# Performance work log

Hardware: AMD Instinct MI355X
Metric: run time of the kernel (lower is better)

## Reference

```python
import jax, jax.numpy as jnp
import numpy as np

D_HIDDEN = 400
D_ANCHOR = 31
N_LAYER = 24
N_HEADS = 8
DIM_HEAD = 400
D_INNER = 800
D_STATE = 16
D_CONV = 4
DT_RANK = 25  # ceil(400/16)
PE_HIDDEN = 48
EPS = 1e-5


def _point_embed(x, w, b):
    # Fourier point embedding (3DShape2VecSet PointEmbed), dim-major freq layout.
    d = x.shape[-1]
    nf = PE_HIDDEN // (2 * d)
    freqs = (2.0 ** jnp.arange(nf, dtype=x.dtype)) * jnp.pi  # [nf]
    proj = (x[..., None] * freqs).reshape(*x.shape[:-1], d * nf)  # [b,n,d*nf]
    emb = jnp.concatenate([jnp.sin(proj), jnp.cos(proj), x], axis=-1)  # [b,n,48+d]
    return emb @ w.T + b


def _rmsnorm(x, w):
    return x * jax.lax.rsqrt(jnp.mean(x * x, axis=-1, keepdims=True) + EPS) * w


def _layernorm(x, w, b):
    mu = jnp.mean(x, axis=-1, keepdims=True)
    var = jnp.var(x, axis=-1, keepdims=True)
    return (x - mu) * jax.lax.rsqrt(var + EPS) * w + b


def _selective_scan(u, dt, A, Bm, Cm, Dp):
    # u, dt: [b,l,di]; A: [di,n]; Bm, Cm: [b,l,n]; Dp: [di]
    def step(h, inp):
        u_t, dt_t, B_t, C_t = inp  # [b,di],[b,di],[b,n],[b,n]
        h = jnp.exp(dt_t[..., None] * A) * h + (dt_t * u_t)[..., None] * B_t[:, None, :]
        return h, jnp.einsum('bdn,bn->bd', h, C_t)
    h0 = jnp.zeros((u.shape[0], u.shape[2], A.shape[1]), u.dtype)
    xs = (jnp.swapaxes(u, 0, 1), jnp.swapaxes(dt, 0, 1),
          jnp.swapaxes(Bm, 0, 1), jnp.swapaxes(Cm, 0, 1))
    _, ys = jax.lax.scan(step, h0, xs)
    return jnp.swapaxes(ys, 0, 1) + u * Dp


def _mamba_block(x, norm_w, in_w, conv_w, conv_b, xproj_w, dt_w, dt_b, A_log, Dp, out_w):
    b, L, _ = x.shape
    xn = _rmsnorm(x, norm_w)
    u, z = jnp.split(xn @ in_w.T, 2, axis=-1)  # each [b,L,di]
    # causal depthwise conv1d, kernel D_CONV, left pad D_CONV-1 (torch conv truncated to L)
    u_pad = jnp.pad(u, ((0, 0), (D_CONV - 1, 0), (0, 0)))
    conv = sum(u_pad[:, k:k + L, :] * conv_w[:, k] for k in range(D_CONV)) + conv_b
    u_c = jax.nn.silu(conv)
    dbc = u_c @ xproj_w.T  # [b,L,dt_rank+2n]
    dt, Bm, Cm = jnp.split(dbc, [DT_RANK, DT_RANK + D_STATE], axis=-1)
    dt = jax.nn.softplus(dt @ dt_w.T + dt_b)  # [b,L,di]
    y = _selective_scan(u_c, dt, -jnp.exp(A_log), Bm, Cm, Dp)
    return x + (y * jax.nn.silu(z)) @ out_w.T


def _forward(mash_params, qry, anchor_w, anchor_b, point_w, point_b,
             norm_w, in_w, conv_w, conv_b, xproj_w, dt_w, dt_b, A_log, Dp, out_w,
             ln_q_w, ln_q_b, ln_c_w, ln_c_b, to_q_w, to_kv_w, to_out_w, to_out_b,
             ff_ln_w, ff_ln_b, ff_w1, ff_b1, ff_w2, ff_b2, head_w, head_b):
    # anchor embed on first 6 dims, concat remaining 25 -> [b,na,400]
    anc = _point_embed(mash_params[:, :, :6], anchor_w, anchor_b)
    x = jnp.concatenate([anc, mash_params[:, :, 6:]], axis=-1)
    for i in range(N_LAYER):
        x = _mamba_block(x, norm_w[i], in_w[i], conv_w[i], conv_b[i], xproj_w[i],
                         dt_w[i], dt_b[i], A_log[i], Dp[i], out_w[i])
    q_emb = _point_embed(qry, point_w, point_b)  # [b,nq,400]
    # PreNorm cross-attention (query norm + context norm), no residual
    qn = _layernorm(q_emb, ln_q_w, ln_q_b)
    ctx = _layernorm(x, ln_c_w, ln_c_b)
    b, nq, _ = qn.shape
    na = ctx.shape[1]
    q = (qn @ to_q_w.T).reshape(b, nq, N_HEADS, DIM_HEAD)
    k, v = jnp.split(ctx @ to_kv_w.T, 2, axis=-1)
    k = k.reshape(b, na, N_HEADS, DIM_HEAD)
    v = v.reshape(b, na, N_HEADS, DIM_HEAD)
    sim = jnp.einsum('bihd,bjhd->bhij', q, k) * (DIM_HEAD ** -0.5)
    attn = jax.nn.softmax(sim, axis=-1)
    out = jnp.einsum('bhij,bjhd->bihd', attn, v).reshape(b, nq, N_HEADS * DIM_HEAD)
    latents = out @ to_out_w.T + to_out_b  # [b,nq,400]
    # PreNorm GEGLU FeedForward with residual
    h = _layernorm(latents, ff_ln_w, ff_ln_b) @ ff_w1.T + ff_b1  # [b,nq,3200]
    a, g = jnp.split(h, 2, axis=-1)
    h = (a * jax.nn.gelu(g)) @ ff_w2.T + ff_b2
    latents = latents + h
    occ = (latents @ head_w.T + head_b).squeeze(-1)  # [b,nq]
    return occ


def setup_inputs() -> dict:
    key = jax.random.key(0)
    ks = iter(jax.random.split(key, 48))
    def nrm(shape, scale=0.02):
        return jax.random.normal(next(ks), shape, dtype=jnp.float32) * scale
    B, NA, NQ = 4, 400, 4096
    INNER = N_HEADS * DIM_HEAD  # 3200
    dt_init = jax.random.uniform(next(ks), (N_LAYER, D_INNER), minval=1e-3, maxval=0.1)
    inp = {
        'mash_params': nrm((B, NA, D_ANCHOR), 1.0),
        'qry': jax.random.uniform(next(ks), (B, NQ, 3), minval=-1.0, maxval=1.0),
        'anchor_w': nrm((D_HIDDEN - D_ANCHOR + 6, PE_HIDDEN + 6)),
        'anchor_b': jnp.zeros((D_HIDDEN - D_ANCHOR + 6,), jnp.float32),
        'point_w': nrm((D_HIDDEN, PE_HIDDEN + 3)),
        'point_b': jnp.zeros((D_HIDDEN,), jnp.float32),
        'norm_w': jnp.ones((N_LAYER, D_HIDDEN), jnp.float32),
        'in_w': nrm((N_LAYER, 2 * D_INNER, D_HIDDEN)),
        'conv_w': nrm((N_LAYER, D_INNER, D_CONV), 0.2),
        'conv_b': jnp.zeros((N_LAYER, D_INNER), jnp.float32),
        'xproj_w': nrm((N_LAYER, DT_RANK + 2 * D_STATE, D_INNER)),
        'dt_w': nrm((N_LAYER, D_INNER, DT_RANK), 0.1),
        'dt_b': jnp.log(jnp.expm1(dt_init)),
        'A_log': jnp.log(jnp.broadcast_to(jnp.arange(1, D_STATE + 1, dtype=jnp.float32),
                                          (N_LAYER, D_INNER, D_STATE))),
        'Dp': jnp.ones((N_LAYER, D_INNER), jnp.float32),
        'out_w': nrm((N_LAYER, D_HIDDEN, D_INNER)),
        'ln_q_w': jnp.ones((D_HIDDEN,), jnp.float32), 'ln_q_b': jnp.zeros((D_HIDDEN,), jnp.float32),
        'ln_c_w': jnp.ones((D_HIDDEN,), jnp.float32), 'ln_c_b': jnp.zeros((D_HIDDEN,), jnp.float32),
        'to_q_w': nrm((INNER, D_HIDDEN)),
        'to_kv_w': nrm((2 * INNER, D_HIDDEN)),
        'to_out_w': nrm((D_HIDDEN, INNER)),
        'to_out_b': jnp.zeros((D_HIDDEN,), jnp.float32),
        'ff_ln_w': jnp.ones((D_HIDDEN,), jnp.float32), 'ff_ln_b': jnp.zeros((D_HIDDEN,), jnp.float32),
        'ff_w1': nrm((8 * D_HIDDEN, D_HIDDEN)),
        'ff_b1': jnp.zeros((8 * D_HIDDEN,), jnp.float32),
        'ff_w2': nrm((D_HIDDEN, 4 * D_HIDDEN)),
        'ff_b2': jnp.zeros((D_HIDDEN,), jnp.float32),
        'head_w': nrm((1, D_HIDDEN)),
        'head_b': jnp.zeros((1,), jnp.float32),
    }
    return inp


def reference(mash_params, qry, anchor_w, anchor_b, point_w, point_b,
              norm_w, in_w, conv_w, conv_b, xproj_w, dt_w, dt_b, A_log, Dp, out_w,
              ln_q_w, ln_q_b, ln_c_w, ln_c_b, to_q_w, to_kv_w, to_out_w, to_out_b,
              ff_ln_w, ff_ln_b, ff_w1, ff_b1, ff_w2, ff_b2, head_w, head_b):
    return _forward(mash_params, qry, anchor_w, anchor_b, point_w, point_b,
                    norm_w, in_w, conv_w, conv_b, xproj_w, dt_w, dt_b, A_log, Dp, out_w,
                    ln_q_w, ln_q_b, ln_c_w, ln_c_b, to_q_w, to_kv_w, to_out_w, to_out_b,
                    ff_ln_w, ff_ln_b, ff_w1, ff_b1, ff_w2, ff_b2, head_w, head_b)
```

## Files before the change

### kernel.cpp

```cpp
#include <hip/hip_runtime.h>


#define EPI_NONE 0
#define EPI_SOFTPLUS 1
#define EPI_RES 2
#define EPI_GEGLU 3

typedef short bf16x8 __attribute__((ext_vector_type(8)));
typedef float f32x4 __attribute__((ext_vector_type(4)));

static __device__ __forceinline__ float silu_f(float x) {
  return x / (1.f + __expf(-x));
}
static __device__ __forceinline__ float softplus_f(float x) {
  return fmaxf(x, 0.f) + log1pf(__expf(-fabsf(x)));
}
static __device__ __forceinline__ float gelu_f(float x) {
  const float c = 0.7978845608028654f;
  return 0.5f * x * (1.f + tanhf(c * (x + 0.044715f * x * x * x)));
}
static __device__ __forceinline__ unsigned short f2bf(float f) {
  union { float f; unsigned int u; } v; v.f = f;
  unsigned int r = v.u + 0x7FFFu + ((v.u >> 16) & 1u);
  return (unsigned short)(r >> 16);
}
static __device__ __forceinline__ float bf2f(unsigned short h) {
  union { unsigned int u; float f; } v; v.u = ((unsigned int)h) << 16;
  return v.f;
}

__global__ void cvt_w_kernel(const float* __restrict__ src, unsigned short* __restrict__ dst,
                             int Lr, int R, int C, int Rp, int Cp) {
  size_t i8 = ((size_t)blockIdx.x * 256 + threadIdx.x) * 8;
  size_t total = (size_t)Lr * Rp * Cp;
  if (i8 >= total) return;
  int cp = (int)(i8 % Cp);
  size_t rl = i8 / Cp;
  int r = (int)(rl % Rp);
  int l = (int)(rl / Rp);
  const float* s = src + ((size_t)l * R + r) * C + cp;
  bf16x8 o;
#pragma unroll
  for (int q = 0; q < 8; ++q) {
    float v = (r < R && (cp + q) < C) ? s[q] : 0.f;
    o[q] = (short)f2bf(v);
  }
  *reinterpret_cast<bf16x8*>(dst + i8) = o;
}

__global__ void cvt_headrow_k(const float* __restrict__ src, unsigned short* __restrict__ dst,
                              int HB) {
  size_t i8 = ((size_t)blockIdx.x * 256 + threadIdx.x) * 8;
  size_t total = (size_t)HB * 416 * 416;
  if (i8 >= total) return;
  int c = (int)(i8 % 416);
  int n = (int)(i8 / 416);
  int head = n / 416, r = n % 416;
  const float* s = src + ((size_t)(head * 400 + r)) * 400 + c;
  bf16x8 o;
#pragma unroll
  for (int q = 0; q < 8; ++q) {
    float v = (r < 400 && (c + q) < 400) ? s[q] : 0.f;
    o[q] = (short)f2bf(v);
  }
  *reinterpret_cast<bf16x8*>(dst + i8) = o;
}

__global__ void cvt_colhead_k(const float* __restrict__ src, unsigned short* __restrict__ dst,
                              int HB) {
  size_t i8 = ((size_t)blockIdx.x * 256 + threadIdx.x) * 8;
  size_t total = (size_t)512 * HB * 416;
  if (i8 >= total) return;
  int cp = (int)(i8 % ((size_t)HB * 416));
  int r = (int)(i8 / ((size_t)HB * 416));
  int head = cp / 416, cc = cp % 416;
  bf16x8 o;
#pragma unroll
  for (int q = 0; q < 8; ++q) {
    int c = cc + q;
    float v = (r < 400 && c < 400) ? src[(size_t)r * (HB * 400) + head * 400 + c] : 0.f;
    o[q] = (short)f2bf(v);
  }
  *reinterpret_cast<bf16x8*>(dst + i8) = o;
}

template <int EPI, int OUTBF>
__global__ __launch_bounds__(256) void gemm_bf16_k(
    const unsigned short* __restrict__ A, int lda, long long zsA,
    const unsigned short* __restrict__ W, int ldw, long long zsW,
    const float* __restrict__ bias,
    const float* __restrict__ aux, int ldaux,
    void* __restrict__ Cout, int ldc, long long zsC,
    int M, int N, int K) {
  __shared__ unsigned short As[128 * 32];
  __shared__ unsigned short Bs[128 * 32];
  const int tid = threadIdx.x;
  const int lane = tid & 63;
  const int wid = tid >> 6;
  const int wr = wid >> 1, wc = wid & 1;
  const int m0 = blockIdx.y * 128, n0 = blockIdx.x * 128;
  const long long z = blockIdx.z;
  A += z * zsA;
  W += z * zsW;

  f32x4 acc[4][4];
#pragma unroll
  for (int i = 0; i < 4; ++i)
#pragma unroll
    for (int j = 0; j < 4; ++j) acc[i][j] = (f32x4){0.f, 0.f, 0.f, 0.f};

  const int i0 = tid;
  const int i1 = tid + 256;
  const unsigned short* gA0 = A + (size_t)(m0 + (i0 >> 2)) * lda + ((i0 & 3) << 3);
  const unsigned short* gA1 = A + (size_t)(m0 + (i1 >> 2)) * lda + ((i1 & 3) << 3);
  const unsigned short* gB0 = W + (size_t)(n0 + (i0 >> 2)) * ldw + ((i0 & 3) << 3);
  const unsigned short* gB1 = W + (size_t)(n0 + (i1 >> 2)) * ldw + ((i1 & 3) << 3);
  unsigned short* lA0 = &As[i0 * 8];
  unsigned short* lA1 = &As[i1 * 8];
  unsigned short* lB0 = &Bs[i0 * 8];
  unsigned short* lB1 = &Bs[i1 * 8];

  const int fr = lane & 15, fq = lane >> 4;
  const int arow = wr * 64 + fr;
  const int brow = wc * 64 + fr;

  for (int k0 = 0; k0 < K; k0 += 32) {
    __builtin_amdgcn_global_load_lds(
        (const __attribute__((address_space(1))) unsigned int*)(gA0 + k0),
        (__attribute__((address_space(3))) unsigned int*)lA0, 16, 0, 0);
    __builtin_amdgcn_global_load_lds(
        (const __attribute__((address_space(1))) unsigned int*)(gA1 + k0),
        (__attribute__((address_space(3))) unsigned int*)lA1, 16, 0, 0);
    __builtin_amdgcn_global_load_lds(
        (const __attribute__((address_space(1))) unsigned int*)(gB0 + k0),
        (__attribute__((address_space(3))) unsigned int*)lB0, 16, 0, 0);
    __builtin_amdgcn_global_load_lds(
        (const __attribute__((address_space(1))) unsigned int*)(gB1 + k0),
        (__attribute__((address_space(3))) unsigned int*)lB1, 16, 0, 0);
    __syncthreads();
    bf16x8 av[4], bv[4];
#pragma unroll
    for (int mi = 0; mi < 4; ++mi)
      av[mi] = *reinterpret_cast<const bf16x8*>(&As[(arow + mi * 16) * 32 + fq * 8]);
#pragma unroll
    for (int ni = 0; ni < 4; ++ni)
      bv[ni] = *reinterpret_cast<const bf16x8*>(&Bs[(brow + ni * 16) * 32 + fq * 8]);
#pragma unroll
    for (int mi = 0; mi < 4; ++mi)
#pragma unroll
      for (int ni = 0; ni < 4; ++ni)
        acc[mi][ni] =
            __builtin_amdgcn_mfma_f32_16x16x32_bf16(av[mi], bv[ni], acc[mi][ni], 0, 0, 0);
    __syncthreads();
  }

  float* Cf = (float*)Cout + z * zsC;
  unsigned short* Cb = (unsigned short*)Cout + z * zsC;
  const float* auxp = aux ? aux + z * zsC : aux;
#pragma unroll
  for (int mi = 0; mi < 4; ++mi) {
#pragma unroll
    for (int r = 0; r < 4; ++r) {
      int m = m0 + wr * 64 + mi * 16 + fq * 4 + r;
      if (m >= M) continue;
#pragma unroll
      for (int ni = 0; ni < 4; ++ni) {
        int n = n0 + wc * 64 + ni * 16 + fr;
        if (n >= N) continue;
        float v = acc[mi][ni][r];
        if (bias) v += bias[n];
        if (EPI == EPI_GEGLU) v = auxp[(size_t)m * ldaux + n] * gelu_f(v);
        else if (EPI == EPI_RES) v += auxp[(size_t)m * ldaux + n];
        if (OUTBF) Cb[(size_t)m * ldc + n] = f2bf(v);
        else Cf[(size_t)m * ldc + n] = v;
      }
    }
  }
}

template <int BM, int BN, int BK, int TM, int TN, int EPI>
__global__ __launch_bounds__(256) void gemm_k(
    const float* __restrict__ A, int lda,
    const float* __restrict__ W, int ldw,
    const float* __restrict__ bias,
    float* __restrict__ C, int ldc,
    int M, int N, int K) {
  __shared__ float As[BK][BM];
  __shared__ float Bs[BK][BN];
  const int tid = threadIdx.x;
  const int tx = tid % (BN / TN);
  const int ty = tid / (BN / TN);
  const int m0 = blockIdx.y * BM;
  const int n0 = blockIdx.x * BN;

  float acc[TM][TN];
#pragma unroll
  for (int i = 0; i < TM; ++i)
#pragma unroll
    for (int j = 0; j < TN; ++j) acc[i][j] = 0.f;

  const int a_row = (tid * 4) / BK;
  const int a_col = (tid * 4) % BK;

  for (int k0 = 0; k0 < K; k0 += BK) {
    {
      int gm = m0 + a_row, gk = k0 + a_col;
      float4 v = make_float4(0.f, 0.f, 0.f, 0.f);
      if (gm < M) {
        if (gk + 3 < K) {
          v = *reinterpret_cast<const float4*>(A + (size_t)gm * lda + gk);
        } else {
          float tmp[4];
#pragma unroll
          for (int q = 0; q < 4; ++q)
            tmp[q] = (gk + q < K) ? A[(size_t)gm * lda + gk + q] : 0.f;
          v = make_float4(tmp[0], tmp[1], tmp[2], tmp[3]);
        }
      }
      As[a_col + 0][a_row] = v.x;
      As[a_col + 1][a_row] = v.y;
      As[a_col + 2][a_row] = v.z;
      As[a_col + 3][a_row] = v.w;
    }
    {
      int gn = n0 + a_row, gk = k0 + a_col;
      float4 v = make_float4(0.f, 0.f, 0.f, 0.f);
      if (gn < N) {
        if (gk + 3 < K) {
          v = *reinterpret_cast<const float4*>(W + (size_t)gn * ldw + gk);
        } else {
          float tmp[4];
#pragma unroll
          for (int q = 0; q < 4; ++q)
            tmp[q] = (gk + q < K) ? W[(size_t)gn * ldw + gk + q] : 0.f;
          v = make_float4(tmp[0], tmp[1], tmp[2], tmp[3]);
        }
      }
      Bs[a_col + 0][a_row] = v.x;
      Bs[a_col + 1][a_row] = v.y;
      Bs[a_col + 2][a_row] = v.z;
      Bs[a_col + 3][a_row] = v.w;
    }
    __syncthreads();
#pragma unroll
    for (int kk = 0; kk < BK; ++kk) {
      float a[TM], bb[TN];
#pragma unroll
      for (int i = 0; i < TM; i += 4)
        *reinterpret_cast<float4*>(&a[i]) =
            *reinterpret_cast<const float4*>(&As[kk][ty * TM + i]);
#pragma unroll
      for (int j = 0; j < TN; j += 4)
        *reinterpret_cast<float4*>(&bb[j]) =
            *reinterpret_cast<const float4*>(&Bs[kk][tx * TN + j]);
#pragma unroll
      for (int i = 0; i < TM; ++i)
#pragma unroll
        for (int j = 0; j < TN; ++j) acc[i][j] = fmaf(a[i], bb[j], acc[i][j]);
    }
    __syncthreads();
  }

#pragma unroll
  for (int i = 0; i < TM; ++i) {
    int m = m0 + ty * TM + i;
    if (m >= M) continue;
#pragma unroll
    for (int j = 0; j < TN; ++j) {
      int n = n0 + tx * TN + j;
      if (n >= N) continue;
      float v = acc[i][j];
      if (bias) v += bias[n];
      if (EPI == EPI_SOFTPLUS) v = softplus_f(v);
      C[(size_t)m * ldc + n] = v;
    }
  }
}

__global__ void anchor_embed_kernel(const float* __restrict__ mash,
                                    float* __restrict__ aemb) {
  int row = blockIdx.x;
  int lane = threadIdx.x;
  if (lane >= 54) return;
  const float PI = 3.14159265358979323846f;
  float e;
  if (lane < 48) {
    int j = (lane < 24) ? lane : lane - 24;
    int d = j >> 2, f = j & 3;
    float v = mash[row * 31 + d] * (PI * (float)(1 << f));
    e = (lane < 24) ? sinf(v) : cosf(v);
  } else {
    e = mash[row * 31 + (lane - 48)];
  }
  aemb[row * 54 + lane] = e;
}

__global__ void point_embed_q_kernel(const float* __restrict__ qry,
                                     unsigned short* __restrict__ qep) {
  int row = blockIdx.x;
  int lane = threadIdx.x;
  const float PI = 3.14159265358979323846f;
  float e = 0.f;
  if (lane < 48) {
    int j = (lane < 24) ? lane : lane - 24;
    int d = j >> 3, f = j & 7;
    float v = qry[row * 3 + d] * (PI * (float)(1 << f));
    e = (lane < 24) ? sinf(v) : cosf(v);
  } else if (lane < 51) {
    e = qry[row * 3 + (lane - 48)];
  }
  qep[(size_t)row * 64 + lane] = f2bf(e);
}

__global__ void copy_tail_kernel(const float* __restrict__ mash,
                                 float* __restrict__ x) {
  int idx = blockIdx.x * 256 + threadIdx.x;
  if (idx >= 1600 * 25) return;
  int row = idx / 25, j = idx % 25;
  x[row * 400 + 375 + j] = mash[row * 31 + 6 + j];
}

__global__ void rmsnorm_bf16_kernel(const float* __restrict__ x,
                                    const float* __restrict__ w,
                                    unsigned short* __restrict__ out) {
  int row = blockIdx.x;
  int lane = threadIdx.x;
  float ss = 0.f;
  float vals[7];
  int nv = 0;
  for (int c = lane; c < 400; c += 64) {
    float v = x[(size_t)row * 400 + c];
    vals[nv++] = v;
    ss += v * v;
  }
#pragma unroll
  for (int off = 1; off < 64; off <<= 1) ss += __shfl_xor(ss, off);
  float r = rsqrtf(ss * (1.f / 400.f) + 1e-5f);
  nv = 0;
  for (int c = lane; c < 416; c += 64) {
    unsigned short o = 0;
    if (c < 400) o = f2bf(vals[nv++] * r * w[c]);
    out[(size_t)row * 416 + c] = o;
  }
}

__global__ void layernorm_bf16_kernel(const float* __restrict__ x,
                                      const float* __restrict__ w,
                                      const float* __restrict__ b,
                                      unsigned short* __restrict__ out) {
  int row = blockIdx.x;
  int lane = threadIdx.x;
  float s = 0.f, s2 = 0.f;
  float vals[7];
  int nv = 0;
  for (int c = lane; c < 400; c += 64) {
    float v = x[(size_t)row * 400 + c];
    vals[nv++] = v;
    s += v;
    s2 += v * v;
  }
#pragma unroll
  for (int off = 1; off < 64; off <<= 1) {
    s += __shfl_xor(s, off);
    s2 += __shfl_xor(s2, off);
  }
  float mu = s * (1.f / 400.f);
  float var = s2 * (1.f / 400.f) - mu * mu;
  float r = rsqrtf(var + 1e-5f);
  nv = 0;
  for (int c = lane; c < 416; c += 64) {
    unsigned short o = 0;
    if (c < 400) o = f2bf((vals[nv++] - mu) * r * w[c] + b[c]);
    out[(size_t)row * 416 + c] = o;
  }
}

__global__ void conv_silu_kernel(const float* __restrict__ uz,
                                 const float* __restrict__ cw,
                                 const float* __restrict__ cb,
                                 unsigned short* __restrict__ ucb,
                                 float* __restrict__ uc32) {
  int idx = blockIdx.x * 256 + threadIdx.x;
  if (idx >= 1600 * 800) return;
  int c = idx % 800;
  int row = idx / 800;
  int l = row % 400;
  int b = row / 400;
  float acc = cb[c];
  float w0 = cw[c * 4 + 0], w1 = cw[c * 4 + 1], w2 = cw[c * 4 + 2], w3 = cw[c * 4 + 3];
  const float* ub = uz + (size_t)b * 400 * 1600 + c;
  if (l >= 3) acc += ub[(size_t)(l - 3) * 1600] * w0;
  if (l >= 2) acc += ub[(size_t)(l - 2) * 1600] * w1;
  if (l >= 1) acc += ub[(size_t)(l - 1) * 1600] * w2;
  acc += ub[(size_t)l * 1600] * w3;
  float v = silu_f(acc);
  uc32[idx] = v;
  ucb[(size_t)row * 800 + c] = f2bf(v);
}

__global__ void scan_kernel(const float* __restrict__ uc,
                            const float* __restrict__ dt,
                            const float* __restrict__ dbc,
                            const float* __restrict__ uz,
                            const float* __restrict__ A_log,
                            const float* __restrict__ Dp,
                            unsigned short* __restrict__ gb) {
  int t = blockIdx.x * 256 + threadIdx.x;
  if (t >= 12800) return;
  int g = t & 3;
  int bd = t >> 2;
  int b = bd / 800;
  int d = bd - b * 800;
  float A0 = -__expf(A_log[d * 16 + g * 4 + 0]);
  float A1 = -__expf(A_log[d * 16 + g * 4 + 1]);
  float A2 = -__expf(A_log[d * 16 + g * 4 + 2]);
  float A3 = -__expf(A_log[d * 16 + g * 4 + 3]);
  float Dpd = Dp[d];
  float h0 = 0.f, h1 = 0.f, h2 = 0.f, h3 = 0.f;
  const int off = 25 + g * 4;
  for (int l0 = 0; l0 < 400; l0 += 4) {
    float dtv[4], uv[4], zv[4], Bv[4][4], Cv[4][4];
#pragma unroll
    for (int q = 0; q < 4; ++q) {
      size_t base = (size_t)(b * 400 + l0 + q);
      dtv[q] = dt[base * 800 + d];
      uv[q] = uc[base * 800 + d];
      zv[q] = uz[base * 1600 + 800 + d];
      const float* bc = dbc + base * 57 + off;
#pragma unroll
      for (int s = 0; s < 4; ++s) {
        Bv[q][s] = bc[s];
        Cv[q][s] = bc[16 + s];
      }
    }
#pragma unroll
    for (int q = 0; q < 4; ++q) {
      float du = dtv[q] * uv[q];
      h0 = __expf(dtv[q] * A0) * h0 + du * Bv[q][0];
      h1 = __expf(dtv[q] * A1) * h1 + du * Bv[q][1];
      h2 = __expf(dtv[q] * A2) * h2 + du * Bv[q][2];
      h3 = __expf(dtv[q] * A3) * h3 + du * Bv[q][3];
      float yv = h0 * Cv[q][0] + h1 * Cv[q][1] + h2 * Cv[q][2] + h3 * Cv[q][3];
      yv += __shfl_xor(yv, 1);
      yv += __shfl_xor(yv, 2);
      if (g == 0) {
        size_t base = (size_t)(b * 400 + l0 + q);
        gb[base * 800 + d] = f2bf((yv + uv[q] * Dpd) * silu_f(zv[q]));
      }
    }
  }
}

__global__ void softmax_k(float* S) {
  int row = blockIdx.x * 4 + (threadIdx.x >> 6);
  int lane = threadIdx.x & 63;
  float* sr = S + (size_t)row * 416;
  float v[7];
  float m = -1e30f;
#pragma unroll
  for (int i = 0; i < 7; ++i) {
    int c = lane + i * 64;
    v[i] = (c < 400) ? sr[c] : -1e30f;
    m = fmaxf(m, v[i]);
  }
#pragma unroll
  for (int off = 1; off < 64; off <<= 1) m = fmaxf(m, __shfl_xor(m, off));
  float sum = 0.f;
#pragma unroll
  for (int i = 0; i < 7; ++i) {
    int c = lane + i * 64;
    float p = (c < 400) ? __expf(0.05f * (v[i] - m)) : 0.f;
    v[i] = p;
    sum += p;
  }
#pragma unroll
  for (int off = 1; off < 64; off <<= 1) sum += __shfl_xor(sum, off);
  float inv = 1.f / sum;
  unsigned short* pr = (unsigned short*)sr;
#pragma unroll
  for (int i = 0; i < 7; ++i) {
    int c = lane + i * 64;
    if (c < 400) pr[c] = f2bf(v[i] * inv);
    else if (c < 416) pr[c] = 0;
  }
}

__global__ void vt_repack_k(const unsigned short* __restrict__ kvp,
                            unsigned short* __restrict__ vt, int h) {
  __shared__ unsigned short tbuf[32][66];
  int tid = threadIdx.x;
  int b = blockIdx.z;
  int j0 = blockIdx.x * 32, d0 = blockIdx.y * 64;
  for (int idx = tid; idx < 32 * 64; idx += 256) {
    int j = idx >> 6, dd = idx & 63;
    unsigned short val = 0;
    if (j0 + j < 400 && d0 + dd < 400)
      val = kvp[(size_t)(b * 400 + j0 + j) * 6656 + 3328 + h * 416 + d0 + dd];
    tbuf[j][dd] = val;
  }
  __syncthreads();
  for (int idx = tid; idx < 64 * 32; idx += 256) {
    int dd = idx >> 5, j = idx & 31;
    vt[(size_t)(b * 512 + d0 + dd) * 416 + j0 + j] = tbuf[j][dd];
  }
}

__global__ void head_kernel(const float* __restrict__ lat,
                            const float* __restrict__ hw,
                            const float* __restrict__ hb,
                            float* __restrict__ out) {
  int row = blockIdx.x * 4 + (threadIdx.x >> 6);
  int lane = threadIdx.x & 63;
  float s = 0.f;
  for (int c = lane; c < 400; c += 64) s += lat[(size_t)row * 400 + c] * hw[c];
#pragma unroll
  for (int off = 1; off < 64; off <<= 1) s += __shfl_xor(s, off);
  if (lane == 0) out[row] = s + hb[0];
}

static inline int cdiv(int a, int b) { return (a + b - 1) / b; }
static inline int cvtblocks(long long elems) { return (int)((elems / 8 + 255) / 256); }

extern "C" void kernel_launch(void* const* d_in, const int* in_sizes, int n_in,
                              void* d_out, int out_size, void* d_ws, size_t ws_size,
                              hipStream_t stream) {
  (void)in_sizes; (void)n_in; (void)out_size;

  const float* mash     = (const float*)d_in[0];
  const float* qry      = (const float*)d_in[1];
  const float* anchor_w = (const float*)d_in[2];
  const float* anchor_b = (const float*)d_in[3];
  const float* point_w  = (const float*)d_in[4];
  const float* point_b  = (const float*)d_in[5];
  const float* norm_w   = (const float*)d_in[6];
  const float* in_w     = (const float*)d_in[7];
  const float* conv_w   = (const float*)d_in[8];
  const float* conv_b   = (const float*)d_in[9];
  const float* xproj_w  = (const float*)d_in[10];
  const float* dt_w     = (const float*)d_in[11];
  const float* dt_b     = (const float*)d_in[12];
  const float* A_log    = (const float*)d_in[13];
  const float* Dp       = (const float*)d_in[14];
  const float* out_w    = (const float*)d_in[15];
  const float* ln_q_w   = (const float*)d_in[16];
  const float* ln_q_b   = (const float*)d_in[17];
  const float* ln_c_w   = (const float*)d_in[18];
  const float* ln_c_b   = (const float*)d_in[19];
  const float* to_q_w   = (const float*)d_in[20];
  const float* to_kv_w  = (const float*)d_in[21];
  const float* to_out_w = (const float*)d_in[22];
  const float* to_out_b = (const float*)d_in[23];
  const float* ff_ln_w  = (const float*)d_in[24];
  const float* ff_ln_b  = (const float*)d_in[25];
  const float* ff_w1    = (const float*)d_in[26];
  const float* ff_b1    = (const float*)d_in[27];
  const float* ff_w2    = (const float*)d_in[28];
  const float* ff_b2    = (const float*)d_in[29];
  const float* head_w   = (const float*)d_in[30];
  const float* head_b   = (const float*)d_in[31];

  const size_t WI   = 0;
  const size_t WX   = 8306688;
  const size_t WO   = 9535488;
  const size_t WKV  = 14450688;
  const size_t WP   = 15835136;
  const size_t WQ   = 15851520;
  const size_t WTO  = 16570368;
  const size_t WF1  = 17422336;
  const size_t WF2  = 18101248;
  const size_t XOFF = 18510848;
  const size_t LATO = 19150848;
  const size_t P    = 25704448;
  const size_t QEMB = 0;
  const size_t SOFF = 0;
  const size_t CTX  = 6815744;
  const size_t QH   = 6815744;
  const size_t VT   = 10223616;
  const size_t QEP  = 10650112;
  const size_t FFA  = 0;
  const size_t XNB  = P + 0;
  const size_t UZ   = P + 346112;
  const size_t UCB  = P + 2906112;
  const size_t UC32 = P + 3571712;
  const size_t DTO  = P + 4851712;
  const size_t DBC  = P + 6131712;
  const size_t GB   = P + 6222912;
  const size_t AEMB = P + 6888512;
  const size_t QN   = P + 0;
  const size_t KVP  = P + 3407872;
  const size_t LNL  = P + 0;
  const size_t FFG  = P + 3407872;
  const size_t TOTAL = P + 9158656;

  if (ws_size < TOTAL * sizeof(float)) return;

  float* ws = (float*)d_ws;
  float* X   = ws + XOFF;
  float* LAT = ws + LATO;
  unsigned short* pWI  = (unsigned short*)(ws + WI);
  unsigned short* pWX  = (unsigned short*)(ws + WX);
  unsigned short* pWO  = (unsigned short*)(ws + WO);
  unsigned short* pWKV = (unsigned short*)(ws + WKV);
  unsigned short* pWP  = (unsigned short*)(ws + WP);
  unsigned short* pWQ  = (unsigned short*)(ws + WQ);
  unsigned short* pWTO = (unsigned short*)(ws + WTO);
  unsigned short* pWF1 = (unsigned short*)(ws + WF1);
  unsigned short* pWF2 = (unsigned short*)(ws + WF2);

  cvt_w_kernel<<<cvtblocks(24LL*1664*416), 256, 0, stream>>>(in_w,   pWI, 24, 1600, 400, 1664, 416);
  cvt_w_kernel<<<cvtblocks(24LL*128*800),  256, 0, stream>>>(xproj_w,pWX, 24, 57,   800, 128,  800);
  cvt_w_kernel<<<cvtblocks(24LL*512*800),  256, 0, stream>>>(out_w,  pWO, 24, 400,  800, 512,  800);
  cvt_headrow_k<<<cvtblocks(16LL*416*416), 256, 0, stream>>>(to_kv_w, pWKV, 16);
  cvt_w_kernel<<<cvtblocks(512LL*64),      256, 0, stream>>>(point_w, pWP, 1, 400, 51, 512, 64);
  cvt_headrow_k<<<cvtblocks(8LL*416*416),  256, 0, stream>>>(to_q_w, pWQ, 8);
  cvt_colhead_k<<<cvtblocks(512LL*8*416),  256, 0, stream>>>(to_out_w, pWTO, 8);
  cvt_w_kernel<<<cvtblocks(3264LL*416),    256, 0, stream>>>(ff_w1, pWF1, 1, 3200, 400, 3264, 416);
  cvt_w_kernel<<<cvtblocks(512LL*1600),    256, 0, stream>>>(ff_w2, pWF2, 1, 400, 1600, 512, 1600);

  anchor_embed_kernel<<<1600, 64, 0, stream>>>(mash, ws + AEMB);
  gemm_k<64, 64, 16, 4, 4, EPI_NONE><<<dim3(6, 25), 256, 0, stream>>>(
      ws + AEMB, 54, anchor_w, 54, anchor_b, X, 400, 1600, 375, 54);
  copy_tail_kernel<<<cdiv(1600 * 25, 256), 256, 0, stream>>>(mash, X);

  for (int L = 0; L < 24; ++L) {
    rmsnorm_bf16_kernel<<<1600, 64, 0, stream>>>(X, norm_w + (size_t)L * 400,
                                                 (unsigned short*)(ws + XNB));
    gemm_bf16_k<EPI_NONE, 0><<<dim3(13, 13), 256, 0, stream>>>(
        (unsigned short*)(ws + XNB), 416, 0, pWI + (size_t)L * 1664 * 416, 416, 0,
        nullptr, nullptr, 0, ws + UZ, 1600, 0, 1600, 1600, 416);
    conv_silu_kernel<<<cdiv(1600 * 800, 256), 256, 0, stream>>>(
        ws + UZ, conv_w + (size_t)L * 3200, conv_b + (size_t)L * 800,
        (unsigned short*)(ws + UCB), ws + UC32);
    gemm_bf16_k<EPI_NONE, 0><<<dim3(1, 13), 256, 0, stream>>>(
        (unsigned short*)(ws + UCB), 800, 0, pWX + (size_t)L * 128 * 800, 800, 0,
        nullptr, nullptr, 0, ws + DBC, 57, 0, 1600, 57, 800);
    gemm_k<64, 64, 16, 4, 4, EPI_SOFTPLUS><<<dim3(13, 25), 256, 0, stream>>>(
        ws + DBC, 57, dt_w + (size_t)L * 800 * 25, 25, dt_b + (size_t)L * 800,
        ws + DTO, 800, 1600, 800, 25);
    scan_kernel<<<50, 256, 0, stream>>>(ws + UC32, ws + DTO, ws + DBC, ws + UZ,
                                        A_log + (size_t)L * 12800,
                                        Dp + (size_t)L * 800,
                                        (unsigned short*)(ws + GB));
    gemm_bf16_k<EPI_RES, 0><<<dim3(4, 13), 256, 0, stream>>>(
        (unsigned short*)(ws + GB), 800, 0, pWO + (size_t)L * 512 * 800, 800, 0,
        nullptr, X, 400, X, 400, 0, 1600, 400, 800);
  }

  layernorm_bf16_kernel<<<1600, 64, 0, stream>>>(X, ln_c_w, ln_c_b,
                                                 (unsigned short*)(ws + CTX));
  gemm_bf16_k<EPI_NONE, 1><<<dim3(52, 13), 256, 0, stream>>>(
      (unsigned short*)(ws + CTX), 416, 0, pWKV, 416, 0, nullptr, nullptr, 0,
      (unsigned short*)(ws + KVP), 6656, 0, 1600, 6656, 416);

  point_embed_q_kernel<<<16384, 64, 0, stream>>>(qry, (unsigned short*)(ws + QEP));
  gemm_bf16_k<EPI_NONE, 0><<<dim3(4, 128), 256, 0, stream>>>(
      (unsigned short*)(ws + QEP), 64, 0, pWP, 64, 0, point_b, nullptr, 0,
      ws + QEMB, 400, 0, 16384, 400, 64);
  layernorm_bf16_kernel<<<16384, 64, 0, stream>>>(ws + QEMB, ln_q_w, ln_q_b,
                                                  (unsigned short*)(ws + QN));

  for (int h = 0; h < 8; ++h) {
    vt_repack_k<<<dim3(13, 8, 4), 256, 0, stream>>>(
        (unsigned short*)(ws + KVP), (unsigned short*)(ws + VT), h);
    gemm_bf16_k<EPI_NONE, 1><<<dim3(4, 128), 256, 0, stream>>>(
        (unsigned short*)(ws + QN), 416, 0, pWQ + (size_t)h * 416 * 416, 416, 0,
        nullptr, nullptr, 0, (unsigned short*)(ws + QH), 416, 0, 16384, 416, 416);
    gemm_bf16_k<EPI_NONE, 0><<<dim3(4, 32, 4), 256, 0, stream>>>(
        (unsigned short*)(ws + QH), 416, 4096LL * 416,
        (unsigned short*)(ws + KVP) + (size_t)h * 416, 6656, 400LL * 6656,
        nullptr, nullptr, 0, ws + SOFF, 416, 4096LL * 416, 4096, 400, 416);
    softmax_k<<<4096, 256, 0, stream>>>(ws + SOFF);
    gemm_bf16_k<EPI_NONE, 1><<<dim3(4, 32, 4), 256, 0, stream>>>(
        (unsigned short*)(ws + SOFF), 832, 4096LL * 832,
        (unsigned short*)(ws + VT), 416, 512LL * 416,
        nullptr, nullptr, 0, (unsigned short*)(ws + QH), 416, 4096LL * 416,
        4096, 400, 416);
    if (h == 0) {
      gemm_bf16_k<EPI_NONE, 0><<<dim3(4, 128), 256, 0, stream>>>(
          (unsigned short*)(ws + QH), 416, 0, pWTO + (size_t)h * 416, 3328, 0,
          to_out_b, nullptr, 0, LAT, 400, 0, 16384, 400, 416);
    } else {
      gemm_bf16_k<EPI_RES, 0><<<dim3(4, 128), 256, 0, stream>>>(
          (unsigned short*)(ws + QH), 416, 0, pWTO + (size_t)h * 416, 3328, 0,
          nullptr, LAT, 400, LAT, 400, 0, 16384, 400, 416);
    }
  }

  layernorm_bf16_kernel<<<16384, 64, 0, stream>>>(LAT, ff_ln_w, ff_ln_b,
                                                  (unsigned short*)(ws + LNL));
  for (int bb = 0; bb < 4; ++bb) {
    unsigned short* lnb = (unsigned short*)(ws + LNL) + (size_t)bb * 4096 * 416;
    float* latb = LAT + (size_t)bb * 4096 * 400;
    gemm_bf16_k<EPI_NONE, 0><<<dim3(13, 32), 256, 0, stream>>>(
        lnb, 416, 0, pWF1, 416, 0, ff_b1, nullptr, 0, ws + FFA, 1600, 0,
        4096, 1600, 416);
    gemm_bf16_k<EPI_GEGLU, 1><<<dim3(13, 32), 256, 0, stream>>>(
        lnb, 416, 0, pWF1 + (size_t)1600 * 416, 416, 0, ff_b1 + 1600,
        ws + FFA, 1600, (unsigned short*)(ws + FFG), 1600, 0, 4096, 1600, 416);
    gemm_bf16_k<EPI_RES, 0><<<dim3(4, 32), 256, 0, stream>>>(
        (unsigned short*)(ws + FFG), 1600, 0, pWF2, 1600, 0, ff_b2, latb, 400,
        latb, 400, 0, 4096, 400, 1600);
  }

  head_kernel<<<4096, 256, 0, stream>>>(LAT, head_w, head_b, (float*)d_out);
}
```

Measured before the change: 7.995 ms.

## Restructure cross-attention per batch with head-batched GEMMs and fused output projection

The cross-attention loop now runs per batch element instead of per head. Each iteration does one head-batched Q projection, then QK^T, softmax and PV batched across all eight heads over two row halves. It finishes with a single output projection over the concatenated heads (K=3328), which replaces eight residual-accumulating GEMMs. K and V are projected by separate GEMMs and V is transposed once for all heads. The dbc row stride is padded to 64, and the conv+SiLU kernel is vectorised to process four channels per thread. The workspace layout grows to hold the larger per-head buffers, and the launches change shape.

Result: no change. 8.044 ms (+0.6%).

```diff
diff --git a/kernel.cpp b/kernel.cpp
--- a/kernel.cpp
+++ b/kernel.cpp
@@ -380,22 +380,35 @@
                                  const float* __restrict__ cb,
                                  unsigned short* __restrict__ ucb,
                                  float* __restrict__ uc32) {
-  int idx = blockIdx.x * 256 + threadIdx.x;
+  int idx = (blockIdx.x * 256 + threadIdx.x) * 4;
   if (idx >= 1600 * 800) return;
   int c = idx % 800;
   int row = idx / 800;
   int l = row % 400;
   int b = row / 400;
-  float acc = cb[c];
-  float w0 = cw[c * 4 + 0], w1 = cw[c * 4 + 1], w2 = cw[c * 4 + 2], w3 = cw[c * 4 + 3];
   const float* ub = uz + (size_t)b * 400 * 1600 + c;
-  if (l >= 3) acc += ub[(size_t)(l - 3) * 1600] * w0;
-  if (l >= 2) acc += ub[(size_t)(l - 2) * 1600] * w1;
-  if (l >= 1) acc += ub[(size_t)(l - 1) * 1600] * w2;
-  acc += ub[(size_t)l * 1600] * w3;
-  float v = silu_f(acc);
-  uc32[idx] = v;
-  ucb[(size_t)row * 800 + c] = f2bf(v);
+  float4 acc = *reinterpret_cast<const float4*>(cb + c);
+  float wk[4][4];
+#pragma unroll
+  for (int i = 0; i < 4; ++i) {
+    float4 t = *reinterpret_cast<const float4*>(cw + (size_t)(c + i) * 4);
+    wk[i][0] = t.x; wk[i][1] = t.y; wk[i][2] = t.z; wk[i][3] = t.w;
+  }
+#pragma unroll
+  for (int k = 0; k < 4; ++k) {
+    int ls = l - 3 + k;
+    if (ls < 0) continue;
+    float4 u = *reinterpret_cast<const float4*>(ub + (size_t)ls * 1600);
+    acc.x = fmaf(u.x, wk[0][k], acc.x);
+    acc.y = fmaf(u.y, wk[1][k], acc.y);
+    acc.z = fmaf(u.z, wk[2][k], acc.z);
+    acc.w = fmaf(u.w, wk[3][k], acc.w);
+  }
+  float4 v = make_float4(silu_f(acc.x), silu_f(acc.y), silu_f(acc.z), silu_f(acc.w));
+  *reinterpret_cast<float4*>(uc32 + idx) = v;
+  union { unsigned short s[4]; uint2 u; } o;
+  o.s[0] = f2bf(v.x); o.s[1] = f2bf(v.y); o.s[2] = f2bf(v.z); o.s[3] = f2bf(v.w);
+  *reinterpret_cast<uint2*>(ucb + idx) = o.u;
 }
 
 __global__ void scan_kernel(const float* __restrict__ uc,
@@ -426,7 +439,7 @@
       dtv[q] = dt[base * 800 + d];
       uv[q] = uc[base * 800 + d];
       zv[q] = uz[base * 1600 + 800 + d];
-      const float* bc = dbc + base * 57 + off;
+      const float* bc = dbc + base * 64 + off;
 #pragma unroll
       for (int s = 0; s < 4; ++s) {
         Bv[q][s] = bc[s];
@@ -485,23 +498,23 @@
   }
 }
 
-__global__ void vt_repack_k(const unsigned short* __restrict__ kvp,
-                            unsigned short* __restrict__ vt, int h) {
+__global__ void vt_repack_k(const unsigned short* __restrict__ vb,
+                            unsigned short* __restrict__ vt) {
   __shared__ unsigned short tbuf[32][66];
   int tid = threadIdx.x;
-  int b = blockIdx.z;
+  int b = blockIdx.z >> 3, h = blockIdx.z & 7;
   int j0 = blockIdx.x * 32, d0 = blockIdx.y * 64;
   for (int idx = tid; idx < 32 * 64; idx += 256) {
     int j = idx >> 6, dd = idx & 63;
     unsigned short val = 0;
     if (j0 + j < 400 && d0 + dd < 400)
-      val = kvp[(size_t)(b * 400 + j0 + j) * 6656 + 3328 + h * 416 + d0 + dd];
+      val = vb[(size_t)(b * 400 + j0 + j) * 3328 + h * 416 + d0 + dd];
     tbuf[j][dd] = val;
   }
   __syncthreads();
   for (int idx = tid; idx < 64 * 32; idx += 256) {
     int dd = idx >> 5, j = idx & 31;
-    vt[(size_t)(b * 512 + d0 + dd) * 416 + j0 + j] = tbuf[j][dd];
+    vt[((size_t)(b * 8 + h) * 512 + d0 + dd) * 416 + j0 + j] = tbuf[j][dd];
   }
 }
 
@@ -562,35 +575,37 @@
   const size_t WI   = 0;
   const size_t WX   = 8306688;
   const size_t WO   = 9535488;
-  const size_t WKV  = 14450688;
+  const size_t WK   = 14450688;
+  const size_t WV   = 15142912;
   const size_t WP   = 15835136;
   const size_t WQ   = 15851520;
-  const size_t WTO  = 16570368;
-  const size_t WF1  = 17422336;
-  const size_t WF2  = 18101248;
-  const size_t XOFF = 18510848;
-  const size_t LATO = 19150848;
-  const size_t P    = 25704448;
+  const size_t WTO  = 16543744;
+  const size_t WF1  = 17395712;
+  const size_t WF2  = 18074624;
+  const size_t XOFF = 18484224;
+  const size_t LATO = 19124224;
+  const size_t P    = 25677824;
   const size_t QEMB = 0;
+  const size_t VB   = 0;
+  const size_t QEP  = 6553600;
   const size_t SOFF = 0;
-  const size_t CTX  = 6815744;
-  const size_t QH   = 6815744;
-  const size_t VT   = 10223616;
-  const size_t QEP  = 10650112;
-  const size_t FFA  = 0;
+  const size_t QH8  = 6815744;
   const size_t XNB  = P + 0;
   const size_t UZ   = P + 346112;
   const size_t UCB  = P + 2906112;
   const size_t UC32 = P + 3571712;
   const size_t DTO  = P + 4851712;
   const size_t DBC  = P + 6131712;
-  const size_t GB   = P + 6222912;
-  const size_t AEMB = P + 6888512;
-  const size_t QN   = P + 0;
-  const size_t KVP  = P + 3407872;
+  const size_t GB   = P + 6234112;
+  const size_t AEMB = P + 6899712;
+  const size_t KB   = P + 0;
+  const size_t QN   = P + 2662400;
+  const size_t VT8  = P + 6070272;
+  const size_t OB   = P + 9478144;
   const size_t LNL  = P + 0;
-  const size_t FFG  = P + 3407872;
-  const size_t TOTAL = P + 9158656;
+  const size_t FFA  = P + 3407872;
+  const size_t FFG  = P + 9961472;
+  const size_t TOTAL = P + 16293888;
 
   if (ws_size < TOTAL * sizeof(float)) return;
 
@@ -600,7 +615,8 @@
   unsigned short* pWI  = (unsigned short*)(ws + WI);
   unsigned short* pWX  = (unsigned short*)(ws + WX);
   unsigned short* pWO  = (unsigned short*)(ws + WO);
-  unsigned short* pWKV = (unsigned short*)(ws + WKV);
+  unsigned short* pWK  = (unsigned short*)(ws + WK);
+  unsigned short* pWV  = (unsigned short*)(ws + WV);
   unsigned short* pWP  = (unsigned short*)(ws + WP);
   unsigned short* pWQ  = (unsigned short*)(ws + WQ);
   unsigned short* pWTO = (unsigned short*)(ws + WTO);
@@ -610,7 +626,8 @@
   cvt_w_kernel<<<cvtblocks(24LL*1664*416), 256, 0, stream>>>(in_w,   pWI, 24, 1600, 400, 1664, 416);
   cvt_w_kernel<<<cvtblocks(24LL*128*800),  256, 0, stream>>>(xproj_w,pWX, 24, 57,   800, 128,  800);
   cvt_w_kernel<<<cvtblocks(24LL*512*800),  256, 0, stream>>>(out_w,  pWO, 24, 400,  800, 512,  800);
-  cvt_headrow_k<<<cvtblocks(16LL*416*416), 256, 0, stream>>>(to_kv_w, pWKV, 16);
+  cvt_headrow_k<<<cvtblocks(8LL*416*416),  256, 0, stream>>>(to_kv_w, pWK, 8);
+  cvt_headrow_k<<<cvtblocks(8LL*416*416),  256, 0, stream>>>(to_kv_w + 3200LL*400, pWV, 8);
   cvt_w_kernel<<<cvtblocks(512LL*64),      256, 0, stream>>>(point_w, pWP, 1, 400, 51, 512, 64);
   cvt_headrow_k<<<cvtblocks(8LL*416*416),  256, 0, stream>>>(to_q_w, pWQ, 8);
   cvt_colhead_k<<<cvtblocks(512LL*8*416),  256, 0, stream>>>(to_out_w, pWTO, 8);
@@ -628,14 +645,14 @@
     gemm_bf16_k<EPI_NONE, 0><<<dim3(13, 13), 256, 0, stream>>>(
         (unsigned short*)(ws + XNB), 416, 0, pWI + (size_t)L * 1664 * 416, 416, 0,
         nullptr, nullptr, 0, ws + UZ, 1600, 0, 1600, 1600, 416);
-    conv_silu_kernel<<<cdiv(1600 * 800, 256), 256, 0, stream>>>(
+    conv_silu_kernel<<<1250, 256, 0, stream>>>(
         ws + UZ, conv_w + (size_t)L * 3200, conv_b + (size_t)L * 800,
         (unsigned short*)(ws + UCB), ws + UC32);
     gemm_bf16_k<EPI_NONE, 0><<<dim3(1, 13), 256, 0, stream>>>(
         (unsigned short*)(ws + UCB), 800, 0, pWX + (size_t)L * 128 * 800, 800, 0,
-        nullptr, nullptr, 0, ws + DBC, 57, 0, 1600, 57, 800);
+        nullptr, nullptr, 0, ws + DBC, 64, 0, 1600, 57, 800);
     gemm_k<64, 64, 16, 4, 4, EPI_SOFTPLUS><<<dim3(13, 25), 256, 0, stream>>>(
-        ws + DBC, 57, dt_w + (size_t)L * 800 * 25, 25, dt_b + (size_t)L * 800,
+        ws + DBC, 64, dt_w + (size_t)L * 800 * 25, 25, dt_b + (size_t)L * 800,
         ws + DTO, 800, 1600, 800, 25);
     scan_kernel<<<50, 256, 0, stream>>>(ws + UC32, ws + DTO, ws + DBC, ws + UZ,
                                         A_log + (size_t)L * 12800,
@@ -646,11 +663,16 @@
         nullptr, X, 400, X, 400, 0, 1600, 400, 800);
   }
 
-  layernorm_bf16_kernel<<<1600, 64, 0, stream>>>(X, ln_c_w, ln_c_b,
-                                                 (unsigned short*)(ws + CTX));
-  gemm_bf16_k<EPI_NONE, 1><<<dim3(52, 13), 256, 0, stream>>>(
-      (unsigned short*)(ws + CTX), 416, 0, pWKV, 416, 0, nullptr, nullptr, 0,
-      (unsigned short*)(ws + KVP), 6656, 0, 1600, 6656, 416);
+  unsigned short* CTX = (unsigned short*)(ws + OB);
+  layernorm_bf16_kernel<<<1600, 64, 0, stream>>>(X, ln_c_w, ln_c_b, CTX);
+  gemm_bf16_k<EPI_NONE, 1><<<dim3(26, 13), 256, 0, stream>>>(
+      CTX, 416, 0, pWK, 416, 0, nullptr, nullptr, 0,
+      (unsigned short*)(ws + KB), 3328, 0, 1600, 3328, 416);
+  gemm_bf16_k<EPI_NONE, 1><<<dim3(26, 13), 256, 0, stream>>>(
+      CTX, 416, 0, pWV, 416, 0, nullptr, nullptr, 0,
+      (unsigned short*)(ws + VB), 3328, 0, 1600, 3328, 416);
+  vt_repack_k<<<dim3(13, 8, 32), 256, 0, stream>>>(
+      (unsigned short*)(ws + VB), (unsigned short*)(ws + VT8));
 
   point_embed_q_kernel<<<16384, 64, 0, stream>>>(qry, (unsigned short*)(ws + QEP));
   gemm_bf16_k<EPI_NONE, 0><<<dim3(4, 128), 256, 0, stream>>>(
@@ -659,31 +681,29 @@
   layernorm_bf16_kernel<<<16384, 64, 0, stream>>>(ws + QEMB, ln_q_w, ln_q_b,
                                                   (unsigned short*)(ws + QN));
 
-  for (int h = 0; h < 8; ++h) {
-    vt_repack_k<<<dim3(13, 8, 4), 256, 0, stream>>>(
-        (unsigned short*)(ws + KVP), (unsigned short*)(ws + VT), h);
-    gemm_bf16_k<EPI_NONE, 1><<<dim3(4, 128), 256, 0, stream>>>(
-        (unsigned short*)(ws + QN), 416, 0, pWQ + (size_t)h * 416 * 416, 416, 0,
-        nullptr, nullptr, 0, (unsigned short*)(ws + QH), 416, 0, 16384, 416, 416);
-    gemm_bf16_k<EPI_NONE, 0><<<dim3(4, 32, 4), 256, 0, stream>>>(
-        (unsigned short*)(ws + QH), 416, 4096LL * 416,
-        (unsigned short*)(ws + KVP) + (size_t)h * 416, 6656, 400LL * 6656,
-        nullptr, nullptr, 0, ws + SOFF, 416, 4096LL * 416, 4096, 400, 416);
-    softmax_k<<<4096, 256, 0, stream>>>(ws + SOFF);
-    gemm_bf16_k<EPI_NONE, 1><<<dim3(4, 32, 4), 256, 0, stream>>>(
-        (unsigned short*)(ws + SOFF), 832, 4096LL * 832,
-        (unsigned short*)(ws + VT), 416, 512LL * 416,
-        nullptr, nullptr, 0, (unsigned short*)(ws + QH), 416, 4096LL * 416,
-        4096, 400, 416);
-    if (h == 0) {
-      gemm_bf16_k<EPI_NONE, 0><<<dim3(4, 128), 256, 0, stream>>>(
-          (unsigned short*)(ws + QH), 416, 0, pWTO + (size_t)h * 416, 3328, 0,
-          to_out_b, nullptr, 0, LAT, 400, 0, 16384, 400, 416);
-    } else {
-      gemm_bf16_k<EPI_RES, 0><<<dim3(4, 128), 256, 0, stream>>>(
-          (unsigned short*)(ws + QH), 416, 0, pWTO + (size_t)h * 416, 3328, 0,
-          nullptr, LAT, 400, LAT, 400, 0, 16384, 400, 416);
+  for (int b = 0; b < 4; ++b) {
+    gemm_bf16_k<EPI_NONE, 1><<<dim3(4, 32, 8), 256, 0, stream>>>(
+        (unsigned short*)(ws + QN) + (size_t)b * 4096 * 416, 416, 0,
+        pWQ, 416, 416LL * 416, nullptr, nullptr, 0,
+        (unsigned short*)(ws + QH8), 416, 4096LL * 416, 4096, 416, 416);
+    for (int half = 0; half < 2; ++half) {
+      const unsigned short* Aq =
+          (unsigned short*)(ws + QH8) + (size_t)half * 2048 * 416;
+      gemm_bf16_k<EPI_NONE, 0><<<dim3(4, 16, 8), 256, 0, stream>>>(
+          Aq, 416, 4096LL * 416,
+          (unsigned short*)(ws + KB) + (size_t)b * 400 * 3328, 3328, 416LL,
+          nullptr, nullptr, 0, ws + SOFF, 416, 2048LL * 416, 2048, 400, 416);
+      softmax_k<<<4096, 256, 0, stream>>>(ws + SOFF);
+      gemm_bf16_k<EPI_NONE, 1><<<dim3(4, 16, 8), 256, 0, stream>>>(
+          (unsigned short*)(ws + SOFF), 832, 2048LL * 832,
+          (unsigned short*)(ws + VT8) + (size_t)b * 8 * 512 * 416, 416, 512LL * 416,
+          nullptr, nullptr, 0,
+          (unsigned short*)(ws + OB) + (size_t)half * 2048 * 3328, 3328, 416LL,
+          2048, 416, 416);
     }
+    gemm_bf16_k<EPI_NONE, 0><<<dim3(4, 32), 256, 0, stream>>>(
+        (unsigned short*)(ws + OB), 3328, 0, pWTO, 3328, 0, to_out_b, nullptr, 0,
+        LAT + (size_t)b * 4096 * 400, 400, 0, 4096, 400, 3328);
   }
 
   layernorm_bf16_kernel<<<16384, 64, 0, stream>>>(LAT, ff_ln_w, ff_ln_b,
```
